# Kernel optimization log

Hardware: AMD Instinct MI355X
Metric: run time of the kernel (lower is better)

Reference implementation:

```python
import jax, jax.numpy as jnp
import numpy as np
from jax import lax

N = 8000
SEQ = 200
MAX_STEPS = 199  # tf.less(i, 199)


def setup_inputs() -> dict:
    key = jax.random.key(0)
    k1, k2, k3, k4 = jax.random.split(key, 4)
    a = jax.random.randint(k1, (SEQ,), 0, N, dtype=jnp.int32)
    s = jax.random.bernoulli(k2, 0.5, (SEQ,)).astype(jnp.float32)
    # original inits pe/ne as identity and kp as zeros; use small random tables
    # so the loss/grads are non-trivial, plus the identity structure on the diag
    pe = jnp.eye(N, dtype=jnp.float32) + 0.01 * jax.random.normal(k3, (N, N), dtype=jnp.float32)
    ne = jnp.eye(N, dtype=jnp.float32) + 0.01 * jax.random.normal(k4, (N, N), dtype=jnp.float32)
    kp = jnp.zeros((N,), dtype=jnp.float32)
    return {"a": a, "s": s, "pe": pe, "ne": ne, "kp": kp}


def _regularizer(t):
    return jnp.sum(jnp.log(jnp.abs(t) + 1.0))


def reference(a, s, pe, ne, kp):
    # Early-stop semantics of the tf.while_loop: step i runs iff all s[0..i] >= 0
    # and i < 199. Express as a masked lax.scan of fixed length MAX_STEPS.
    valid = jnp.cumprod((s[:MAX_STEPS] >= 0).astype(kp.dtype))  # [199]

    def step(carry, inp):
        k, l = carry
        ai, si, m = inp
        p = jnp.clip(k[ai], 0.01, 0.99)
        li = -(si * jnp.log(p) + (1.0 - si) * jnp.log(1.0 - p))
        l = l + m * li
        k_new = jnp.clip(k + si * pe[ai] + (1.0 - si) * ne[ai], -30.0, 30.0)
        k = jnp.where(m > 0, k_new, k)
        return (k, l), None

    (_, loss), _ = lax.scan(step, (kp, jnp.float32(0.0)),
                            (a[:MAX_STEPS], s[:MAX_STEPS], valid))
    total = loss + 0.5 * (_regularizer(pe) + _regularizer(ne))
    return total
```

## Files before the change

kernel.cpp:

```cpp
#include <hip/hip_runtime.h>

#define N 8000
#define SEQ 200
#define MAX_STEPS 199

#define REG_THREADS 256
#define SB 1472
#define CB 576
#define ST (SB * REG_THREADS)
#define CT (CB * REG_THREADS)
#define NN4 16000000
#define S1 11520000
#define SFULL 30
#define CFULL 30

typedef float f4 __attribute__((ext_vector_type(4)));

__device__ __forceinline__ float log_sum4(f4 v) {
    return __log2f(fabsf(v[0]) + 1.0f) + __log2f(fabsf(v[1]) + 1.0f) +
           __log2f(fabsf(v[2]) + 1.0f) + __log2f(fabsf(v[3]) + 1.0f);
}

__global__ void k_init_gather(const int* __restrict__ a,
                              const float* __restrict__ s,
                              const float* __restrict__ pe,
                              const float* __restrict__ ne,
                              float* __restrict__ D, int useD,
                              float* __restrict__ out) {
    if (blockIdx.x == 0 && threadIdx.x == 0) out[0] = 0.0f;
    if (!useD) return;

    __shared__ int   sa[MAX_STEPS];
    __shared__ float ss[MAX_STEPS];
    for (int i = threadIdx.x; i < MAX_STEPS; i += blockDim.x) {
        sa[i] = a[i];
        ss[i] = s[i];
    }
    __syncthreads();

    int idx = blockIdx.x * blockDim.x + threadIdx.x;
    const int total = MAX_STEPS * MAX_STEPS;
    if (idx < total) {
        int t = idx / MAX_STEPS;
        int i = idx - t * MAX_STEPS;
        float st = ss[t];
        size_t off = (size_t)sa[t] * N + (size_t)sa[i];
        float d = st * pe[off] + (1.0f - st) * ne[off];
        D[idx] = d;
    }
}

__global__ void __launch_bounds__(REG_THREADS)
k_fused(const int* __restrict__ a,
        const float* __restrict__ s,
        const float* __restrict__ pe,
        const float* __restrict__ ne,
        const float* __restrict__ kp,
        const float* __restrict__ D, int useD,
        float* __restrict__ out) {
    __shared__ float wsum[REG_THREADS / 64];
    const int tid = threadIdx.x;

    if (blockIdx.x == 0) {
        __shared__ int   sa[MAX_STEPS];
        __shared__ float ss[MAX_STEPS];
        for (int i = tid; i < MAX_STEPS; i += REG_THREADS) {
            sa[i] = a[i];
            ss[i] = s[i];
        }
        __syncthreads();

        __shared__ int V;
        if (tid == 0) {
            int v = MAX_STEPS;
            for (int t = 0; t < MAX_STEPS; ++t)
                if (ss[t] < 0.0f) { v = t; break; }
            V = v;
        }
        __syncthreads();

        float li = 0.0f;
        if (tid < MAX_STEPS && tid < V) {
            int j = sa[tid];
            float k = kp[j];
            if (useD) {
                int t = 0;
                for (; t + 8 <= tid; t += 8) {
                    float d[8];
                    #pragma unroll
                    for (int u = 0; u < 8; ++u) d[u] = D[(t + u) * MAX_STEPS + tid];
                    #pragma unroll
                    for (int u = 0; u < 8; ++u)
                        k = fminf(fmaxf(k + d[u], -30.0f), 30.0f);
                }
                for (; t < tid; ++t) {
                    float d = D[t * MAX_STEPS + tid];
                    k = fminf(fmaxf(k + d, -30.0f), 30.0f);
                }
            } else {
                for (int t = 0; t < tid; ++t) {
                    float st = ss[t];
                    size_t off = (size_t)sa[t] * N + (size_t)j;
                    float d = st * pe[off] + (1.0f - st) * ne[off];
                    k = fminf(fmaxf(k + d, -30.0f), 30.0f);
                }
            }
            float p = fminf(fmaxf(k, 0.01f), 0.99f);
            li = -(ss[tid] * logf(p) + (1.0f - ss[tid]) * logf(1.0f - p));
        }

        #pragma unroll
        for (int o = 32; o > 0; o >>= 1) li += __shfl_down(li, o);
        if ((tid & 63) == 0) wsum[tid >> 6] = li;
        __syncthreads();
        if (tid == 0) {
            float total = 0.0f;
            #pragma unroll
            for (int w = 0; w < REG_THREADS / 64; ++w) total += wsum[w];
            atomicAdd(out, total);
        }
        return;
    }

    const f4* __restrict__ pe4 = (const f4*)pe;
    const f4* __restrict__ ne4 = (const f4*)ne;
    const int rb = (int)blockIdx.x - 1;

    float acc = 0.0f;

    if (rb < SB) {
        const int rt = rb * REG_THREADS + tid;
        #pragma unroll 2
        for (int k = 0; k < SFULL; ++k) {
            size_t p = (size_t)rt + (size_t)k * ST;
            f4 v = __builtin_nontemporal_load(&pe4[p]);
            f4 w = __builtin_nontemporal_load(&ne4[p]);
            acc += log_sum4(v);
            acc += log_sum4(w);
        }
        {
            size_t p = (size_t)rt + (size_t)SFULL * ST;
            if (p < (size_t)S1) {
                f4 v = __builtin_nontemporal_load(&pe4[p]);
                f4 w = __builtin_nontemporal_load(&ne4[p]);
                acc += log_sum4(v);
                acc += log_sum4(w);
            }
        }
    } else {
        const int rt = (rb - SB) * REG_THREADS + tid;
        #pragma unroll 2
        for (int k = 0; k < CFULL; ++k) {
            size_t p = (size_t)S1 + (size_t)rt + (size_t)k * CT;
            f4 v = pe4[p];
            f4 w = ne4[p];
            acc += log_sum4(v);
            acc += log_sum4(w);
        }
        {
            size_t p = (size_t)S1 + (size_t)rt + (size_t)CFULL * CT;
            if (p < (size_t)NN4) {
                f4 v = pe4[p];
                f4 w = ne4[p];
                acc += log_sum4(v);
                acc += log_sum4(w);
            }
        }
    }

    #pragma unroll
    for (int o = 32; o > 0; o >>= 1) acc += __shfl_down(acc, o);
    if ((tid & 63) == 0) wsum[tid >> 6] = acc;
    __syncthreads();
    if (tid == 0) {
        float b = 0.0f;
        #pragma unroll
        for (int w = 0; w < REG_THREADS / 64; ++w) b += wsum[w];
        atomicAdd(out, 0.34657359027997264f * b);
    }
}

extern "C" void kernel_launch(void* const* d_in, const int* in_sizes, int n_in,
                              void* d_out, int out_size, void* d_ws, size_t ws_size,
                              hipStream_t stream) {
    const int*   a  = (const int*)d_in[0];
    const float* s  = (const float*)d_in[1];
    const float* pe = (const float*)d_in[2];
    const float* ne = (const float*)d_in[3];
    const float* kp = (const float*)d_in[4];
    float* out = (float*)d_out;

    float* D = (float*)d_ws;
    int useD = (ws_size >= sizeof(float) * MAX_STEPS * MAX_STEPS) ? 1 : 0;

    const int gatherBlocks = (MAX_STEPS * MAX_STEPS + 255) / 256;
    k_init_gather<<<gatherBlocks, 256, 0, stream>>>(a, s, pe, ne, D, useD, out);
    k_fused<<<SB + CB + 1, REG_THREADS, 0, stream>>>(a, s, pe, ne, kp, D, useD, out);
}
```

Before: 86.54 us.

## Fuse gather and regularizer into one kernel with atomic-counter handoff

Replaces the separate gather kernel with one launch. The first blocks build the D gather table and signal completion through an atomic counter, while block 0 spins until that table is ready. The partial sums now go into a workspace accumulator, and the last block to finish writes the output, which removes the second kernel launch and its inter-kernel gap. In exchange it adds a memset launch, relies on all gather blocks being co-resident with block 0 so the spin wait cannot deadlock, and adds atomic traffic at completion.

```diff
diff --git a/kernel.cpp b/kernel.cpp
--- a/kernel.cpp
+++ b/kernel.cpp
@@ -3,12 +3,15 @@
 #define N 8000
 #define SEQ 200
 #define MAX_STEPS 199
-
-#define REG_THREADS 256
-#define SB 1472
-#define CB 576
-#define ST (SB * REG_THREADS)
-#define CT (CB * REG_THREADS)
+#define DTOT (MAX_STEPS * MAX_STEPS)
+
+#define NTH 256
+#define NBLK 2048
+#define GB 155
+#define SBn 1471
+#define CBn 576
+#define STn (SBn * NTH)
+#define CTn (CBn * NTH)
 #define NN4 16000000
 #define S1 11520000
 #define SFULL 30
@@ -21,53 +24,24 @@
            __log2f(fabsf(v[2]) + 1.0f) + __log2f(fabsf(v[3]) + 1.0f);
 }
 
-__global__ void k_init_gather(const int* __restrict__ a,
-                              const float* __restrict__ s,
-                              const float* __restrict__ pe,
-                              const float* __restrict__ ne,
-                              float* __restrict__ D, int useD,
-                              float* __restrict__ out) {
-    if (blockIdx.x == 0 && threadIdx.x == 0) out[0] = 0.0f;
-    if (!useD) return;
-
-    __shared__ int   sa[MAX_STEPS];
-    __shared__ float ss[MAX_STEPS];
-    for (int i = threadIdx.x; i < MAX_STEPS; i += blockDim.x) {
-        sa[i] = a[i];
-        ss[i] = s[i];
-    }
-    __syncthreads();
-
-    int idx = blockIdx.x * blockDim.x + threadIdx.x;
-    const int total = MAX_STEPS * MAX_STEPS;
-    if (idx < total) {
-        int t = idx / MAX_STEPS;
-        int i = idx - t * MAX_STEPS;
-        float st = ss[t];
-        size_t off = (size_t)sa[t] * N + (size_t)sa[i];
-        float d = st * pe[off] + (1.0f - st) * ne[off];
-        D[idx] = d;
-    }
-}
-
-__global__ void __launch_bounds__(REG_THREADS)
-k_fused(const int* __restrict__ a,
-        const float* __restrict__ s,
-        const float* __restrict__ pe,
-        const float* __restrict__ ne,
-        const float* __restrict__ kp,
-        const float* __restrict__ D, int useD,
-        float* __restrict__ out) {
-    __shared__ float wsum[REG_THREADS / 64];
+
+__global__ void __launch_bounds__(NTH, 8)
+k_one(const int* __restrict__ a,
+      const float* __restrict__ s,
+      const float* __restrict__ pe,
+      const float* __restrict__ ne,
+      const float* __restrict__ kp,
+      unsigned int* __restrict__ wsu,
+      float* __restrict__ out) {
+    float* accf = (float*)(wsu + 2);
+    float* D    = (float*)(wsu + 4);
+    __shared__ float wsum[NTH / 64];
     const int tid = threadIdx.x;
 
     if (blockIdx.x == 0) {
         __shared__ int   sa[MAX_STEPS];
         __shared__ float ss[MAX_STEPS];
-        for (int i = tid; i < MAX_STEPS; i += REG_THREADS) {
-            sa[i] = a[i];
-            ss[i] = s[i];
-        }
+        for (int i = tid; i < MAX_STEPS; i += NTH) { sa[i] = a[i]; ss[i] = s[i]; }
         __syncthreads();
 
         __shared__ int V;
@@ -76,6 +50,9 @@
             for (int t = 0; t < MAX_STEPS; ++t)
                 if (ss[t] < 0.0f) { v = t; break; }
             V = v;
+            while (__hip_atomic_load(&wsu[0], __ATOMIC_ACQUIRE,
+                                     __HIP_MEMORY_SCOPE_AGENT) < (unsigned)GB)
+                __builtin_amdgcn_s_sleep(2);
         }
         __syncthreads();
 
@@ -83,28 +60,17 @@
         if (tid < MAX_STEPS && tid < V) {
             int j = sa[tid];
             float k = kp[j];
-            if (useD) {
-                int t = 0;
-                for (; t + 8 <= tid; t += 8) {
-                    float d[8];
-                    #pragma unroll
-                    for (int u = 0; u < 8; ++u) d[u] = D[(t + u) * MAX_STEPS + tid];
-                    #pragma unroll
-                    for (int u = 0; u < 8; ++u)
-                        k = fminf(fmaxf(k + d[u], -30.0f), 30.0f);
-                }
-                for (; t < tid; ++t) {
-                    float d = D[t * MAX_STEPS + tid];
-                    k = fminf(fmaxf(k + d, -30.0f), 30.0f);
-                }
-            } else {
-                for (int t = 0; t < tid; ++t) {
-                    float st = ss[t];
-                    size_t off = (size_t)sa[t] * N + (size_t)j;
-                    float d = st * pe[off] + (1.0f - st) * ne[off];
-                    k = fminf(fmaxf(k + d, -30.0f), 30.0f);
-                }
+            int t = 0;
+            for (; t + 8 <= tid; t += 8) {
+                float d[8];
+                #pragma unroll
+                for (int u = 0; u < 8; ++u) d[u] = D[(t + u) * MAX_STEPS + tid];
+                #pragma unroll
+                for (int u = 0; u < 8; ++u)
+                    k = fminf(fmaxf(k + d[u], -30.0f), 30.0f);
             }
+            for (; t < tid; ++t)
+                k = fminf(fmaxf(k + D[t * MAX_STEPS + tid], -30.0f), 30.0f);
             float p = fminf(fmaxf(k, 0.01f), 0.99f);
             li = -(ss[tid] * logf(p) + (1.0f - ss[tid]) * logf(1.0f - p));
         }
@@ -116,30 +82,56 @@
         if (tid == 0) {
             float total = 0.0f;
             #pragma unroll
-            for (int w = 0; w < REG_THREADS / 64; ++w) total += wsum[w];
-            atomicAdd(out, total);
+            for (int w = 0; w < NTH / 64; ++w) total += wsum[w];
+            atomicAdd(accf, total);
+            unsigned old = __hip_atomic_fetch_add(&wsu[1], 1u, __ATOMIC_ACQ_REL,
+                                                  __HIP_MEMORY_SCOPE_AGENT);
+            if (old == NBLK - 1)
+                out[0] = __hip_atomic_load(accf, __ATOMIC_RELAXED,
+                                           __HIP_MEMORY_SCOPE_AGENT);
         }
         return;
+    }
+
+    const int rb = (int)blockIdx.x - 1;
+
+    if (rb < GB) {
+        __shared__ int   ga[MAX_STEPS];
+        __shared__ float gs[MAX_STEPS];
+        for (int i = tid; i < MAX_STEPS; i += NTH) { ga[i] = a[i]; gs[i] = s[i]; }
+        __syncthreads();
+        int idx = rb * NTH + tid;
+        if (idx < DTOT) {
+            int t = idx / MAX_STEPS;
+            int i = idx - t * MAX_STEPS;
+            float st = gs[t];
+            size_t off = (size_t)ga[t] * N + (size_t)ga[i];
+            D[idx] = st * pe[off] + (1.0f - st) * ne[off];
+        }
+        __syncthreads();
+        if (tid == 0) {
+            __threadfence();
+            __hip_atomic_fetch_add(&wsu[0], 1u, __ATOMIC_RELEASE,
+                                   __HIP_MEMORY_SCOPE_AGENT);
+        }
     }
 
     const f4* __restrict__ pe4 = (const f4*)pe;
     const f4* __restrict__ ne4 = (const f4*)ne;
-    const int rb = (int)blockIdx.x - 1;
-
     float acc = 0.0f;
 
-    if (rb < SB) {
-        const int rt = rb * REG_THREADS + tid;
+    if (rb < SBn) {
+        const int rt = rb * NTH + tid;
         #pragma unroll 2
         for (int k = 0; k < SFULL; ++k) {
-            size_t p = (size_t)rt + (size_t)k * ST;
+            size_t p = (size_t)rt + (size_t)k * STn;
             f4 v = __builtin_nontemporal_load(&pe4[p]);
             f4 w = __builtin_nontemporal_load(&ne4[p]);
             acc += log_sum4(v);
             acc += log_sum4(w);
         }
         {
-            size_t p = (size_t)rt + (size_t)SFULL * ST;
+            size_t p = (size_t)rt + (size_t)SFULL * STn;
             if (p < (size_t)S1) {
                 f4 v = __builtin_nontemporal_load(&pe4[p]);
                 f4 w = __builtin_nontemporal_load(&ne4[p]);
@@ -148,17 +140,17 @@
             }
         }
     } else {
-        const int rt = (rb - SB) * REG_THREADS + tid;
+        const int rt = (rb - SBn) * NTH + tid;
         #pragma unroll 2
         for (int k = 0; k < CFULL; ++k) {
-            size_t p = (size_t)S1 + (size_t)rt + (size_t)k * CT;
+            size_t p = (size_t)S1 + (size_t)rt + (size_t)k * CTn;
             f4 v = pe4[p];
             f4 w = ne4[p];
             acc += log_sum4(v);
             acc += log_sum4(w);
         }
         {
-            size_t p = (size_t)S1 + (size_t)rt + (size_t)CFULL * CT;
+            size_t p = (size_t)S1 + (size_t)rt + (size_t)CFULL * CTn;
             if (p < (size_t)NN4) {
                 f4 v = pe4[p];
                 f4 w = ne4[p];
@@ -175,9 +167,83 @@
     if (tid == 0) {
         float b = 0.0f;
         #pragma unroll
-        for (int w = 0; w < REG_THREADS / 64; ++w) b += wsum[w];
-        atomicAdd(out, 0.34657359027997264f * b);
-    }
+        for (int w = 0; w < NTH / 64; ++w) b += wsum[w];
+        atomicAdd(accf, 0.34657359027997264f * b);
+        unsigned old = __hip_atomic_fetch_add(&wsu[1], 1u, __ATOMIC_ACQ_REL,
+                                              __HIP_MEMORY_SCOPE_AGENT);
+        if (old == NBLK - 1)
+            out[0] = __hip_atomic_load(accf, __ATOMIC_RELAXED,
+                                       __HIP_MEMORY_SCOPE_AGENT);
+    }
+}
+
+__global__ void fb_gather(const int* __restrict__ a, const float* __restrict__ s,
+                          const float* __restrict__ pe, const float* __restrict__ ne,
+                          float* __restrict__ D, float* __restrict__ out) {
+    if (blockIdx.x == 0 && threadIdx.x == 0) out[0] = 0.0f;
+    __shared__ int sa[MAX_STEPS]; __shared__ float ss[MAX_STEPS];
+    for (int i = threadIdx.x; i < MAX_STEPS; i += blockDim.x) { sa[i]=a[i]; ss[i]=s[i]; }
+    __syncthreads();
+    int idx = blockIdx.x * blockDim.x + threadIdx.x;
+    if (idx < DTOT) {
+        int t = idx / MAX_STEPS, i = idx - t * MAX_STEPS;
+        float st = ss[t];
+        size_t off = (size_t)sa[t] * N + (size_t)sa[i];
+        D[idx] = st * pe[off] + (1.0f - st) * ne[off];
+    }
+}
+
+__global__ void __launch_bounds__(NTH)
+fb_fused(const int* __restrict__ a, const float* __restrict__ s,
+         const float* __restrict__ pe, const float* __restrict__ ne,
+         const float* __restrict__ kp, const float* __restrict__ D,
+         float* __restrict__ out) {
+    __shared__ float wsum[NTH / 64];
+    const int tid = threadIdx.x;
+    if (blockIdx.x == 0) {
+        __shared__ int sa[MAX_STEPS]; __shared__ float ss[MAX_STEPS];
+        for (int i = tid; i < MAX_STEPS; i += NTH) { sa[i]=a[i]; ss[i]=s[i]; }
+        __syncthreads();
+        __shared__ int V;
+        if (tid == 0) { int v=MAX_STEPS; for(int t=0;t<MAX_STEPS;++t) if(ss[t]<0.f){v=t;break;} V=v; }
+        __syncthreads();
+        float li = 0.0f;
+        if (tid < MAX_STEPS && tid < V) {
+            int j = sa[tid]; float k = kp[j];
+            for (int t = 0; t < tid; ++t)
+                k = fminf(fmaxf(k + D[t*MAX_STEPS+tid], -30.0f), 30.0f);
+            float p = fminf(fmaxf(k, 0.01f), 0.99f);
+            li = -(ss[tid]*logf(p) + (1.0f-ss[tid])*logf(1.0f-p));
+        }
+        #pragma unroll
+        for (int o = 32; o > 0; o >>= 1) li += __shfl_down(li, o);
+        if ((tid & 63) == 0) wsum[tid >> 6] = li;
+        __syncthreads();
+        if (tid == 0) { float t2=0; for (int w=0;w<NTH/64;++w) t2+=wsum[w]; atomicAdd(out, t2); }
+        return;
+    }
+    const int rb = (int)blockIdx.x - 1;
+    const f4* pe4 = (const f4*)pe; const f4* ne4 = (const f4*)ne;
+    float acc = 0.0f;
+    const int RT = 2047 * NTH;
+    const int rt = rb * NTH + tid;
+    #pragma unroll 2
+    for (int k = 0; k < 30; ++k) {
+        size_t p = (size_t)rt + (size_t)k * RT;
+        f4 v = __builtin_nontemporal_load(&pe4[p]);
+        f4 w = __builtin_nontemporal_load(&ne4[p]);
+        acc += log_sum4(v); acc += log_sum4(w);
+    }
+    { size_t p = (size_t)rt + (size_t)30 * RT;
+      if (p < (size_t)NN4) { f4 v=__builtin_nontemporal_load(&pe4[p]);
+                             f4 w=__builtin_nontemporal_load(&ne4[p]);
+                             acc += log_sum4(v); acc += log_sum4(w); } }
+    #pragma unroll
+    for (int o = 32; o > 0; o >>= 1) acc += __shfl_down(acc, o);
+    if ((tid & 63) == 0) wsum[tid >> 6] = acc;
+    __syncthreads();
+    if (tid == 0) { float b=0; for (int w=0;w<NTH/64;++w) b+=wsum[w];
+                    atomicAdd(out, 0.34657359027997264f * b); }
 }
 
 extern "C" void kernel_launch(void* const* d_in, const int* in_sizes, int n_in,
@@ -190,10 +256,13 @@
     const float* kp = (const float*)d_in[4];
     float* out = (float*)d_out;
 
-    float* D = (float*)d_ws;
-    int useD = (ws_size >= sizeof(float) * MAX_STEPS * MAX_STEPS) ? 1 : 0;
-
-    const int gatherBlocks = (MAX_STEPS * MAX_STEPS + 255) / 256;
-    k_init_gather<<<gatherBlocks, 256, 0, stream>>>(a, s, pe, ne, D, useD, out);
-    k_fused<<<SB + CB + 1, REG_THREADS, 0, stream>>>(a, s, pe, ne, kp, D, useD, out);
-}
+    if (ws_size >= 16 + sizeof(float) * DTOT) {
+        unsigned int* wsu = (unsigned int*)d_ws;
+        hipMemsetAsync(wsu, 0, 16, stream);
+        k_one<<<NBLK, NTH, 0, stream>>>(a, s, pe, ne, kp, wsu, out);
+    } else if (ws_size >= sizeof(float) * DTOT) {
+        float* D = (float*)d_ws;
+        fb_gather<<<(DTOT + NTH - 1) / NTH, NTH, 0, stream>>>(a, s, pe, ne, D, out);
+        fb_fused<<<2048, NTH, 0, stream>>>(a, s, pe, ne, kp, D, out);
+    }
+}
```

Result: slower. 182.8 us (+111.3%).
